# Kernel tuning notes

Measured on AMD Instinct MI355X. Metric: run time of the kernel, lower is better.

Reference implementation:

```python
import jax, jax.numpy as jnp
import numpy as np

LAMBDA = 0.1   # lambda_ init arg
RHO = 1.0      # ADMM penalty parameter
N_ITERS = 50   # fixed ADMM iteration count (replaces eps_rel/eps_abs stopping rule, jit-friendly)


def _admm_box_qp(Q1, P):
    """Solve, for every (b, n): min_x 0.5 x^T Q1[b] x + P[b,n]^T x  s.t. 0 <= x <= 1.
    Q1: [b, m, m] (shared across n, so factor once per b), P: [b, n, m]. Returns z: [b, n, m]."""
    b, n, m = P.shape
    M_inv = jnp.linalg.inv(Q1 + RHO * jnp.eye(m, dtype=Q1.dtype))  # [b, m, m]

    x0 = jnp.zeros((b, n, m), P.dtype)

    def step(carry, _):
        x, z, u = carry
        rhs = RHO * (z - u) - P                       # [b, n, m]
        x = jnp.einsum('bij,bnj->bni', M_inv, rhs)    # x-update: (Q1 + rho I) x = rhs
        z = jnp.clip(x + u, 0.0, 1.0)                 # z-update: projection onto box [lb, ub] = [0, 1]
        u = u + x - z                                 # dual update
        return (x, z, u), None

    (x, z, u), _ = jax.lax.scan(step, (x0, x0, x0), None, length=N_ITERS)
    return z


def reference(Q, V):
    b, n, d = Q.shape
    m = V.shape[1]
    V = V / m
    # Q1 = 2 V V^T : [b, m, m]
    Q1 = 2.0 * jnp.einsum('bmd,bkd->bmk', V, V)
    # P = -2 V Q^T + lambda/m : [b, n, m]  (avoid materializing the b*n stacked copies of Q1)
    P = -2.0 * jnp.einsum('bmd,bnd->bnm', V, Q) + LAMBDA / m
    x = _admm_box_qp(Q1, P)                           # [b, n, m] in [0, 1]
    xb = jnp.where(x > 0.5, 1.0, 0.0)                 # hard threshold
    coeffs = xb / (jnp.abs(xb).sum(axis=-1, keepdims=True) + 1e-10)
    return jnp.einsum('bnm,bmd->bnd', coeffs, V)


def setup_inputs() -> dict:
    key = jax.random.key(0)
    kq, kv = jax.random.split(key)
    Q = jax.random.normal(kq, (8, 2048, 128), dtype=jnp.float32)
    V = jax.random.normal(kv, (8, 128, 128), dtype=jnp.float32)
    return {"Q": Q, "V": V}
```

## Files before the change

### kernel.cpp

```cpp
#include <hip/hip_runtime.h>

#define NBATCH 8
#define NROWS 2048
#define MDIM 128
#define NITER 50
#define PSTR 65
#define RSTR_R 136
#define WSTR 104
#define XSTR 132

#define RH_B 0
#define RM_B 17408
#define RL_B 34816
#define WH_B 52224
#define WM_B 78848
#define WL_B 105472
#define CNT_B 132096
#define SMEM_BYTES 136192
#define PMAT_B 0
#define QST_B 68608
#define XB_B 0
#define CF_B 36864

typedef unsigned short ushort_t;
typedef __attribute__((ext_vector_type(8))) short bf16x8;
typedef __attribute__((ext_vector_type(8))) unsigned short us8;
typedef __attribute__((ext_vector_type(4))) unsigned short us4;
typedef __attribute__((ext_vector_type(4))) float f32x4;

__device__ __host__ __forceinline__ ushort_t f2bf(float f) {
  unsigned int u = __builtin_bit_cast(unsigned int, f);
  unsigned int r = (u + 0x7fffu + ((u >> 16) & 1u)) >> 16;
  return (ushort_t)r;
}
__device__ __forceinline__ float bf2f(ushort_t h) {
  unsigned int u = ((unsigned int)h) << 16;
  return __builtin_bit_cast(float, u);
}

__global__ __launch_bounds__(256) void mk_m64(const float* __restrict__ V,
                                              double* __restrict__ M,
                                              double* __restrict__ X0) {
  __shared__ double sA[32][130];
  __shared__ double sB[32][130];
  const int b = blockIdx.x >> 4, t = blockIdx.x & 15;
  const int i0 = (t >> 2) << 5, j0 = (t & 3) << 5;
  const float* Vb = V + b * MDIM * MDIM;
  const int tid = threadIdx.x;
  const double S = 1.0 / 128.0;
  for (int idx = tid; idx < 1024; idx += 256) {
    const int r = idx >> 5, c4 = (idx & 31) << 2;
    float4 v = *(const float4*)(Vb + (i0 + r) * MDIM + c4);
    sA[r][c4 + 0] = v.x * S; sA[r][c4 + 1] = v.y * S;
    sA[r][c4 + 2] = v.z * S; sA[r][c4 + 3] = v.w * S;
    float4 w = *(const float4*)(Vb + (j0 + r) * MDIM + c4);
    sB[r][c4 + 0] = w.x * S; sB[r][c4 + 1] = w.y * S;
    sB[r][c4 + 2] = w.z * S; sB[r][c4 + 3] = w.w * S;
  }
  __syncthreads();
  const int tx = tid & 15, ty = tid >> 4;
  double acc[2][2] = {};
  for (int k = 0; k < 128; ++k) {
    double a0 = sA[ty * 2 + 0][k], a1 = sA[ty * 2 + 1][k];
    double b0 = sB[tx * 2 + 0][k], b1 = sB[tx * 2 + 1][k];
    acc[0][0] = fma(a0, b0, acc[0][0]); acc[0][1] = fma(a0, b1, acc[0][1]);
    acc[1][0] = fma(a1, b0, acc[1][0]); acc[1][1] = fma(a1, b1, acc[1][1]);
  }
  double* Mb = M + b * 16384;
  double* Xb = X0 + b * 16384;
#pragma unroll
  for (int i = 0; i < 2; ++i)
#pragma unroll
    for (int j = 0; j < 2; ++j) {
      const int gi = i0 + ty * 2 + i, gj = j0 + tx * 2 + j;
      const double diag = (gi == gj) ? 1.0 : 0.0;
      const double mv = 2.0 * acc[i][j] + diag;
      Mb[gi * 128 + gj] = mv;
      Xb[gi * 128 + gj] = 2.0 * diag - mv;
    }
}

__global__ __launch_bounds__(256) void ns_gemm64(const double* __restrict__ A,
                                                 const double* __restrict__ B,
                                                 double* __restrict__ C,
                                                 const double* __restrict__ Xc,
                                                 int mode) {
  __shared__ double sA[32][130];
  __shared__ double sB[32][130];
  const int b = blockIdx.x >> 4, t = blockIdx.x & 15;
  const int i0 = (t >> 2) << 5, j0 = (t & 3) << 5;
  const double* Ab = A + b * 16384;
  const double* Bb = B + b * 16384;
  const int tid = threadIdx.x;
  for (int idx = tid; idx < 2048; idx += 256) {
    const int r = idx >> 6, c2 = (idx & 63) << 1;
    *(double2*)&sA[r][c2] = *(const double2*)(Ab + (i0 + r) * 128 + c2);
    *(double2*)&sB[r][c2] = *(const double2*)(Bb + (j0 + r) * 128 + c2);
  }
  __syncthreads();
  const int tx = tid & 15, ty = tid >> 4;
  double acc[2][2] = {};
  for (int k = 0; k < 128; ++k) {
    double a0 = sA[ty * 2 + 0][k], a1 = sA[ty * 2 + 1][k];
    double b0 = sB[tx * 2 + 0][k], b1 = sB[tx * 2 + 1][k];
    acc[0][0] = fma(a0, b0, acc[0][0]); acc[0][1] = fma(a0, b1, acc[0][1]);
    acc[1][0] = fma(a1, b0, acc[1][0]); acc[1][1] = fma(a1, b1, acc[1][1]);
  }
  double* Cb = C + b * 16384;
  const double* Xcb = Xc + b * 16384;
#pragma unroll
  for (int i = 0; i < 2; ++i)
#pragma unroll
    for (int j = 0; j < 2; ++j) {
      const int gi = i0 + ty * 2 + i, gj = j0 + tx * 2 + j;
      double v = acc[i][j];
      if (mode != 0) v = 2.0 * Xcb[gi * 128 + gj] - v;
      Cb[gi * 128 + gj] = v;
    }
}

__global__ __launch_bounds__(256) void prep_aux(const double* __restrict__ Minv,
                                                const float* __restrict__ V,
                                                ushort_t* __restrict__ Whg,
                                                ushort_t* __restrict__ Wmg,
                                                ushort_t* __restrict__ Wlg,
                                                double* __restrict__ VsT64) {
  const int b = blockIdx.x >> 3, ch = blockIdx.x & 7;
  const double* Mb = Minv + b * 16384;
  const float* Vb = V + b * 16384;
  ushort_t* Whb = Whg + b * 16384;
  ushort_t* Wmb = Wmg + b * 16384;
  ushort_t* Wlb = Wlg + b * 16384;
  double* Tb = VsT64 + b * 16384;
  const int base = ch * 2048;
  for (int k = threadIdx.x; k < 2048; k += 256) {
    const int idx = base + k;
    const int j = idx >> 7, c = idx & 127;
    const double diag = (j == c) ? 1.0 : 0.0;
    const float wf = (float)(diag - Mb[idx]);
    const ushort_t h = f2bf(wf);
    const float r1 = wf - bf2f(h);
    const ushort_t m_ = f2bf(r1);
    const float r2 = r1 - bf2f(m_);
    const ushort_t l_ = f2bf(r2);
    Whb[c * 128 + j] = h;
    Wmb[c * 128 + j] = m_;
    Wlb[c * 128 + j] = l_;
    Tb[idx] = (double)Vb[c * 128 + j] * (1.0 / 128.0);
  }
}

__global__ __launch_bounds__(1024) void admm_mfma(const float* __restrict__ Q,
                                                  const float* __restrict__ V,
                                                  const ushort_t* __restrict__ Whg,
                                                  const ushort_t* __restrict__ Wmg,
                                                  const ushort_t* __restrict__ Wlg,
                                                  const double* __restrict__ VsT64,
                                                  float* __restrict__ out) {
  __shared__ __align__(16) char smem[SMEM_BYTES];
  const int tid = threadIdx.x;
  const int b = blockIdx.x & 7;
  const int n0 = (blockIdx.x >> 3) << 6;
  const int lane = tid & 63;
  const int w = tid >> 6;
  const int c0_old = w << 3;
  const int c0u = __builtin_amdgcn_readfirstlane(c0_old);
  const int quad = lane >> 4, col16 = lane & 15;
  const int ct = w & 7, nh = w >> 3;
  const int rowA = ct * 16 + col16;
  const int nrow0 = (nh * 2 + 0) * 16 + col16;
  const int nrow1 = (nh * 2 + 1) * 16 + col16;
  const int cbase = ct * 16 + quad * 4;

  const float* Qb = Q + ((size_t)(b * NROWS + n0)) * MDIM;
  const double* Vtc = VsT64 + b * 16384 + c0u;
  const float* Vc = V + b * 16384 + c0u;
  float* outb = out + ((size_t)(b * NROWS + n0)) * MDIM;
  const ushort_t* WG0 = Whg + b * 16384;
  const ushort_t* WG1 = Wmg + b * 16384;
  const ushort_t* WG2 = Wlg + b * 16384;

  float* QST = (float*)(smem + QST_B);
  double* pmat = (double*)(smem + PMAT_B);
  ushort_t* rhp = (ushort_t*)(smem + RH_B);
  ushort_t* rmp = (ushort_t*)(smem + RM_B);
  ushort_t* rlp = (ushort_t*)(smem + RL_B);
  ushort_t* wh = (ushort_t*)(smem + WH_B);
  ushort_t* wm = (ushort_t*)(smem + WM_B);
  ushort_t* wl = (ushort_t*)(smem + WL_B);
  float* sCnt = (float*)(smem + CNT_B);

  for (int idx = tid; idx < 2048; idx += 1024) {
    const int r = idx >> 5, d4 = (idx & 31) << 2;
    const float4 q = *(const float4*)(Qb + r * 128 + d4);
    QST[(d4 + 0) * PSTR + r] = q.x;
    QST[(d4 + 1) * PSTR + r] = q.y;
    QST[(d4 + 2) * PSTR + r] = q.z;
    QST[(d4 + 3) * PSTR + r] = q.w;
  }
  __syncthreads();

  double p8[8];
#pragma unroll
  for (int c = 0; c < 8; ++c) p8[c] = 0.0;
  for (int d = 0; d < 128; ++d) {
    const double a = (double)QST[d * PSTR + lane];
    const double* vt = Vtc + d * 128;
#pragma unroll
    for (int c = 0; c < 8; ++c) p8[c] = fma(a, vt[c], p8[c]);
  }
  const double LAM = 0.1 / 128.0;
#pragma unroll
  for (int c = 0; c < 8; ++c) p8[c] = fma(-2.0, p8[c], LAM);
  __syncthreads();
#pragma unroll
  for (int c = 0; c < 8; ++c) pmat[lane * 128 + c0_old + c] = p8[c];
  __syncthreads();

  double pC[2][4];
#pragma unroll
  for (int i = 0; i < 4; ++i) {
    pC[0][i] = pmat[nrow0 * 128 + cbase + i];
    pC[1][i] = pmat[nrow1 * 128 + cbase + i];
  }
  __syncthreads();

  {
    const ushort_t* wg[3] = {WG0, WG1, WG2};
    ushort_t* wd[3] = {wh, wm, wl};
#pragma unroll
    for (int L = 0; L < 3; ++L)
      for (int idx = tid; idx < 1536; idx += 1024) {
        const int c = idx / 12, t8 = idx - c * 12;
        *(us8*)(wd[L] + c * WSTR + t8 * 8) =
            *(const us8*)(wg[L] + c * 128 + 32 + t8 * 8);
      }
  }
  bf16x8 wf0h = *(const bf16x8*)(WG0 + rowA * 128 + quad * 8);
  bf16x8 wf0m = *(const bf16x8*)(WG1 + rowA * 128 + quad * 8);
  bf16x8 wf0l = *(const bf16x8*)(WG2 + rowA * 128 + quad * 8);
  __syncthreads();

  double z[2][4], u[2][4];
#pragma unroll
  for (int t = 0; t < 2; ++t)
#pragma unroll
    for (int i = 0; i < 4; ++i) { z[t][i] = 0.0; u[t][i] = 0.0; }

  for (int it = 0; it < NITER; ++it) {
#pragma unroll
    for (int t = 0; t < 2; ++t) {
      const int nr = t ? nrow1 : nrow0;
      us4 hh, mm2, ll;
#pragma unroll
      for (int i = 0; i < 4; ++i) {
        const double rv = (z[t][i] - u[t][i]) - pC[t][i];
        const float rf = (float)rv;
        const ushort_t h = f2bf(rf);
        const float r1 = rf - bf2f(h);
        const ushort_t m_ = f2bf(r1);
        const float r2 = r1 - bf2f(m_);
        const ushort_t l_ = f2bf(r2);
        hh[i] = h; mm2[i] = m_; ll[i] = l_;
      }
      *(us4*)(rhp + nr * RSTR_R + cbase) = hh;
      *(us4*)(rmp + nr * RSTR_R + cbase) = mm2;
      *(us4*)(rlp + nr * RSTR_R + cbase) = ll;
    }
    __syncthreads();

    f32x4 acc0 = {0.f, 0.f, 0.f, 0.f};
    f32x4 acc1 = {0.f, 0.f, 0.f, 0.f};
#pragma unroll
    for (int ks = 0; ks < 4; ++ks) {
      bf16x8 ah, am2, al2;
      if (ks == 0) {
        ah = wf0h; am2 = wf0m; al2 = wf0l;
      } else {
        const int ko = (ks - 1) * 32 + quad * 8;
        ah  = *(const bf16x8*)(wh + rowA * WSTR + ko);
        am2 = *(const bf16x8*)(wm + rowA * WSTR + ko);
        al2 = *(const bf16x8*)(wl + rowA * WSTR + ko);
      }
      const int kq = ks * 32 + quad * 8;
      const bf16x8 b0h = *(const bf16x8*)(rhp + nrow0 * RSTR_R + kq);
      const bf16x8 b0m = *(const bf16x8*)(rmp + nrow0 * RSTR_R + kq);
      const bf16x8 b0l = *(const bf16x8*)(rlp + nrow0 * RSTR_R + kq);
      const bf16x8 b1h = *(const bf16x8*)(rhp + nrow1 * RSTR_R + kq);
      const bf16x8 b1m = *(const bf16x8*)(rmp + nrow1 * RSTR_R + kq);
      const bf16x8 b1l = *(const bf16x8*)(rlp + nrow1 * RSTR_R + kq);
      acc0 = __builtin_amdgcn_mfma_f32_16x16x32_bf16(ah,  b0h, acc0, 0, 0, 0);
      acc0 = __builtin_amdgcn_mfma_f32_16x16x32_bf16(ah,  b0m, acc0, 0, 0, 0);
      acc0 = __builtin_amdgcn_mfma_f32_16x16x32_bf16(am2, b0h, acc0, 0, 0, 0);
      acc0 = __builtin_amdgcn_mfma_f32_16x16x32_bf16(am2, b0m, acc0, 0, 0, 0);
      acc0 = __builtin_amdgcn_mfma_f32_16x16x32_bf16(ah,  b0l, acc0, 0, 0, 0);
      acc0 = __builtin_amdgcn_mfma_f32_16x16x32_bf16(al2, b0h, acc0, 0, 0, 0);
      acc1 = __builtin_amdgcn_mfma_f32_16x16x32_bf16(ah,  b1h, acc1, 0, 0, 0);
      acc1 = __builtin_amdgcn_mfma_f32_16x16x32_bf16(ah,  b1m, acc1, 0, 0, 0);
      acc1 = __builtin_amdgcn_mfma_f32_16x16x32_bf16(am2, b1h, acc1, 0, 0, 0);
      acc1 = __builtin_amdgcn_mfma_f32_16x16x32_bf16(am2, b1m, acc1, 0, 0, 0);
      acc1 = __builtin_amdgcn_mfma_f32_16x16x32_bf16(ah,  b1l, acc1, 0, 0, 0);
      acc1 = __builtin_amdgcn_mfma_f32_16x16x32_bf16(al2, b1h, acc1, 0, 0, 0);
    }
    __syncthreads();

#pragma unroll
    for (int t = 0; t < 2; ++t)
#pragma unroll
      for (int i = 0; i < 4; ++i) {
        const float corr = (t == 0) ? acc0[i] : acc1[i];
        const double rv = (z[t][i] - u[t][i]) - pC[t][i];
        const double x = rv - (double)corr;
        const double y = x + u[t][i];
        const double zn = fmin(fmax(y, 0.0), 1.0);
        u[t][i] = y - zn;
        z[t][i] = zn;
      }
  }

  float* xbm = (float*)(smem + XB_B);
#pragma unroll
  for (int t = 0; t < 2; ++t) {
    const int nr = t ? nrow1 : nrow0;
    float4 o;
    o.x = (z[t][0] > 0.5) ? 1.f : 0.f;
    o.y = (z[t][1] > 0.5) ? 1.f : 0.f;
    o.z = (z[t][2] > 0.5) ? 1.f : 0.f;
    o.w = (z[t][3] > 0.5) ? 1.f : 0.f;
    *(float4*)(xbm + nr * XSTR + cbase) = o;
  }
  __syncthreads();

  float xb8[8];
  {
    const float4 a = *(const float4*)(xbm + lane * XSTR + c0_old + 0);
    const float4 c2 = *(const float4*)(xbm + lane * XSTR + c0_old + 4);
    xb8[0] = a.x; xb8[1] = a.y; xb8[2] = a.z; xb8[3] = a.w;
    xb8[4] = c2.x; xb8[5] = c2.y; xb8[6] = c2.z; xb8[7] = c2.w;
  }
  double cnt = 0.0;
#pragma unroll
  for (int c = 0; c < 8; ++c) cnt += (double)xb8[c];
  sCnt[w * 64 + lane] = (float)cnt;
  __syncthreads();
  double k = 0.0;
#pragma unroll
  for (int g = 0; g < 16; ++g) k += (double)sCnt[g * 64 + lane];
  const double rkS = (1.0 / 128.0) / (k + 1e-10);
  float* cf = (float*)(smem + CF_B);
  {
    float4 w0, w1;
    w0.x = (float)((double)xb8[0] * rkS); w0.y = (float)((double)xb8[1] * rkS);
    w0.z = (float)((double)xb8[2] * rkS); w0.w = (float)((double)xb8[3] * rkS);
    w1.x = (float)((double)xb8[4] * rkS); w1.y = (float)((double)xb8[5] * rkS);
    w1.z = (float)((double)xb8[6] * rkS); w1.w = (float)((double)xb8[7] * rkS);
    *(float4*)(cf + lane * XSTR + c0_old + 0) = w0;
    *(float4*)(cf + lane * XSTR + c0_old + 4) = w1;
  }
  __syncthreads();

  float oa[8];
#pragma unroll
  for (int c = 0; c < 8; ++c) oa[c] = 0.f;
#pragma unroll 4
  for (int m4 = 0; m4 < 32; ++m4) {
    const float4 a4 = *(const float4*)(cf + lane * XSTR + (m4 << 2));
    const float* v0 = Vc + ((m4 << 2) + 0) * 128;
    const float* v1 = Vc + ((m4 << 2) + 1) * 128;
    const float* v2 = Vc + ((m4 << 2) + 2) * 128;
    const float* v3 = Vc + ((m4 << 2) + 3) * 128;
#pragma unroll
    for (int c = 0; c < 8; ++c) oa[c] = fmaf(a4.x, v0[c], oa[c]);
#pragma unroll
    for (int c = 0; c < 8; ++c) oa[c] = fmaf(a4.y, v1[c], oa[c]);
#pragma unroll
    for (int c = 0; c < 8; ++c) oa[c] = fmaf(a4.z, v2[c], oa[c]);
#pragma unroll
    for (int c = 0; c < 8; ++c) oa[c] = fmaf(a4.w, v3[c], oa[c]);
  }
#pragma unroll
  for (int q = 0; q < 2; ++q) {
    float4 o;
    o.x = oa[q * 4 + 0]; o.y = oa[q * 4 + 1];
    o.z = oa[q * 4 + 2]; o.w = oa[q * 4 + 3];
    *(float4*)(outb + lane * 128 + c0_old + q * 4) = o;
  }
}

extern "C" void kernel_launch(void* const* d_in, const int* in_sizes, int n_in,
                              void* d_out, int out_size, void* d_ws, size_t ws_size,
                              hipStream_t stream) {
  const float* Q = (const float*)d_in[0];
  const float* V = (const float*)d_in[1];
  float* out = (float*)d_out;
  double* ws = (double*)d_ws;
  double* Mw = ws;
  double* Xa = ws + 131072;
  double* Xb = ws + 262144;
  double* Tw = ws + 393216;

  mk_m64<<<128, 256, 0, stream>>>(V, Mw, Xa);
  double* pa = Xa;
  double* pb = Xb;
  for (int i = 0; i < 3; ++i) {
    ns_gemm64<<<128, 256, 0, stream>>>(pa, Mw, Tw, pa, 0);
    ns_gemm64<<<128, 256, 0, stream>>>(Tw, pa, pb, pa, 1);
    double* tmp = pa; pa = pb; pb = tmp;
  }
  ushort_t* Whg = (ushort_t*)Mw;
  ushort_t* Wmg = Whg + 131072;
  ushort_t* Wlg = Whg + 262144;
  double* VsT64 = Tw;
  prep_aux<<<64, 256, 0, stream>>>(pa, V, Whg, Wmg, Wlg, VsT64);
  admm_mfma<<<256, 1024, 0, stream>>>(Q, V, Whg, Wmg, Wlg, VsT64, out);
}
```

Before: 309.1 us.

## Halve ADMM block rows, keep hi/mid weight fragments in registers, shrink LDS

The main ADMM kernel now processes 32 rows per block with 512 threads (512 blocks), so each wave owns one 16-column tile over both row halves. The hi and mid bf16 weight fragments are held in registers across all k-steps, and only the low part stays in LDS, cutting shared memory from about 136KB to about 55KB so several blocks can share a CU. The small fp64 Newton-Schulz and M-build GEMMs use 16-row tiles with twice as many blocks to fill more CUs. In exchange there is higher register pressure (launch bounds 512,4), less reuse of the A fragments per block, and more redundant weight loads across blocks.

```diff
diff --git a/kernel.cpp b/kernel.cpp
--- a/kernel.cpp
+++ b/kernel.cpp
@@ -4,23 +4,21 @@
 #define NROWS 2048
 #define MDIM 128
 #define NITER 50
-#define PSTR 65
+#define PSTR2 33
 #define RSTR_R 136
-#define WSTR 104
+#define WLSTR 104
 #define XSTR 132
 
 #define RH_B 0
-#define RM_B 17408
-#define RL_B 34816
-#define WH_B 52224
-#define WM_B 78848
-#define WL_B 105472
-#define CNT_B 132096
-#define SMEM_BYTES 136192
+#define RM_B 8704
+#define RL_B 17408
+#define WL_B 26112
+#define CNT_B 52736
+#define SMEM_BYTES 54784
 #define PMAT_B 0
-#define QST_B 68608
+#define QST_B 32768
 #define XB_B 0
-#define CF_B 36864
+#define CF_B 16896
 
 typedef unsigned short ushort_t;
 typedef __attribute__((ext_vector_type(8))) short bf16x8;
@@ -41,43 +39,43 @@
 __global__ __launch_bounds__(256) void mk_m64(const float* __restrict__ V,
                                               double* __restrict__ M,
                                               double* __restrict__ X0) {
-  __shared__ double sA[32][130];
+  __shared__ double sA[16][130];
   __shared__ double sB[32][130];
-  const int b = blockIdx.x >> 4, t = blockIdx.x & 15;
-  const int i0 = (t >> 2) << 5, j0 = (t & 3) << 5;
+  const int b = blockIdx.x >> 5, t = blockIdx.x & 31;
+  const int i0 = (t >> 2) << 4, j0 = (t & 3) << 5;
   const float* Vb = V + b * MDIM * MDIM;
   const int tid = threadIdx.x;
   const double S = 1.0 / 128.0;
-  for (int idx = tid; idx < 1024; idx += 256) {
+  for (int idx = tid; idx < 512; idx += 256) {
     const int r = idx >> 5, c4 = (idx & 31) << 2;
     float4 v = *(const float4*)(Vb + (i0 + r) * MDIM + c4);
     sA[r][c4 + 0] = v.x * S; sA[r][c4 + 1] = v.y * S;
     sA[r][c4 + 2] = v.z * S; sA[r][c4 + 3] = v.w * S;
+  }
+  for (int idx = tid; idx < 1024; idx += 256) {
+    const int r = idx >> 5, c4 = (idx & 31) << 2;
     float4 w = *(const float4*)(Vb + (j0 + r) * MDIM + c4);
     sB[r][c4 + 0] = w.x * S; sB[r][c4 + 1] = w.y * S;
     sB[r][c4 + 2] = w.z * S; sB[r][c4 + 3] = w.w * S;
   }
   __syncthreads();
   const int tx = tid & 15, ty = tid >> 4;
-  double acc[2][2] = {};
+  double acc0 = 0.0, acc1 = 0.0;
   for (int k = 0; k < 128; ++k) {
-    double a0 = sA[ty * 2 + 0][k], a1 = sA[ty * 2 + 1][k];
-    double b0 = sB[tx * 2 + 0][k], b1 = sB[tx * 2 + 1][k];
-    acc[0][0] = fma(a0, b0, acc[0][0]); acc[0][1] = fma(a0, b1, acc[0][1]);
-    acc[1][0] = fma(a1, b0, acc[1][0]); acc[1][1] = fma(a1, b1, acc[1][1]);
+    const double a0 = sA[ty][k];
+    const double b0 = sB[tx * 2 + 0][k], b1 = sB[tx * 2 + 1][k];
+    acc0 = fma(a0, b0, acc0); acc1 = fma(a0, b1, acc1);
   }
   double* Mb = M + b * 16384;
   double* Xb = X0 + b * 16384;
 #pragma unroll
-  for (int i = 0; i < 2; ++i)
-#pragma unroll
-    for (int j = 0; j < 2; ++j) {
-      const int gi = i0 + ty * 2 + i, gj = j0 + tx * 2 + j;
-      const double diag = (gi == gj) ? 1.0 : 0.0;
-      const double mv = 2.0 * acc[i][j] + diag;
-      Mb[gi * 128 + gj] = mv;
-      Xb[gi * 128 + gj] = 2.0 * diag - mv;
-    }
+  for (int j = 0; j < 2; ++j) {
+    const int gi = i0 + ty, gj = j0 + tx * 2 + j;
+    const double diag = (gi == gj) ? 1.0 : 0.0;
+    const double mv = 2.0 * (j ? acc1 : acc0) + diag;
+    Mb[gi * 128 + gj] = mv;
+    Xb[gi * 128 + gj] = 2.0 * diag - mv;
+  }
 }
 
 __global__ __launch_bounds__(256) void ns_gemm64(const double* __restrict__ A,
@@ -85,38 +83,38 @@
                                                  double* __restrict__ C,
                                                  const double* __restrict__ Xc,
                                                  int mode) {
-  __shared__ double sA[32][130];
+  __shared__ double sA[16][130];
   __shared__ double sB[32][130];
-  const int b = blockIdx.x >> 4, t = blockIdx.x & 15;
-  const int i0 = (t >> 2) << 5, j0 = (t & 3) << 5;
+  const int b = blockIdx.x >> 5, t = blockIdx.x & 31;
+  const int i0 = (t >> 2) << 4, j0 = (t & 3) << 5;
   const double* Ab = A + b * 16384;
   const double* Bb = B + b * 16384;
   const int tid = threadIdx.x;
+  for (int idx = tid; idx < 1024; idx += 256) {
+    const int r = idx >> 6, c2 = (idx & 63) << 1;
+    *(double2*)&sA[r][c2] = *(const double2*)(Ab + (i0 + r) * 128 + c2);
+  }
   for (int idx = tid; idx < 2048; idx += 256) {
     const int r = idx >> 6, c2 = (idx & 63) << 1;
-    *(double2*)&sA[r][c2] = *(const double2*)(Ab + (i0 + r) * 128 + c2);
     *(double2*)&sB[r][c2] = *(const double2*)(Bb + (j0 + r) * 128 + c2);
   }
   __syncthreads();
   const int tx = tid & 15, ty = tid >> 4;
-  double acc[2][2] = {};
+  double acc0 = 0.0, acc1 = 0.0;
   for (int k = 0; k < 128; ++k) {
-    double a0 = sA[ty * 2 + 0][k], a1 = sA[ty * 2 + 1][k];
-    double b0 = sB[tx * 2 + 0][k], b1 = sB[tx * 2 + 1][k];
-    acc[0][0] = fma(a0, b0, acc[0][0]); acc[0][1] = fma(a0, b1, acc[0][1]);
-    acc[1][0] = fma(a1, b0, acc[1][0]); acc[1][1] = fma(a1, b1, acc[1][1]);
+    const double a0 = sA[ty][k];
+    const double b0 = sB[tx * 2 + 0][k], b1 = sB[tx * 2 + 1][k];
+    acc0 = fma(a0, b0, acc0); acc1 = fma(a0, b1, acc1);
   }
   double* Cb = C + b * 16384;
   const double* Xcb = Xc + b * 16384;
 #pragma unroll
-  for (int i = 0; i < 2; ++i)
-#pragma unroll
-    for (int j = 0; j < 2; ++j) {
-      const int gi = i0 + ty * 2 + i, gj = j0 + tx * 2 + j;
-      double v = acc[i][j];
-      if (mode != 0) v = 2.0 * Xcb[gi * 128 + gj] - v;
-      Cb[gi * 128 + gj] = v;
-    }
+  for (int j = 0; j < 2; ++j) {
+    const int gi = i0 + ty, gj = j0 + tx * 2 + j;
+    double v = (j ? acc1 : acc0);
+    if (mode != 0) v = 2.0 * Xcb[gi * 128 + gj] - v;
+    Cb[gi * 128 + gj] = v;
+  }
 }
 
 __global__ __launch_bounds__(256) void prep_aux(const double* __restrict__ Minv,
@@ -150,31 +148,30 @@
   }
 }
 
-__global__ __launch_bounds__(1024) void admm_mfma(const float* __restrict__ Q,
-                                                  const float* __restrict__ V,
-                                                  const ushort_t* __restrict__ Whg,
-                                                  const ushort_t* __restrict__ Wmg,
-                                                  const ushort_t* __restrict__ Wlg,
-                                                  const double* __restrict__ VsT64,
-                                                  float* __restrict__ out) {
+__global__ __launch_bounds__(512, 4) void admm_mfma(const float* __restrict__ Q,
+                                                    const float* __restrict__ V,
+                                                    const ushort_t* __restrict__ Whg,
+                                                    const ushort_t* __restrict__ Wmg,
+                                                    const ushort_t* __restrict__ Wlg,
+                                                    const double* __restrict__ VsT64,
+                                                    float* __restrict__ out) {
   __shared__ __align__(16) char smem[SMEM_BYTES];
   const int tid = threadIdx.x;
   const int b = blockIdx.x & 7;
-  const int n0 = (blockIdx.x >> 3) << 6;
+  const int n0 = (blockIdx.x >> 3) << 5;
   const int lane = tid & 63;
   const int w = tid >> 6;
-  const int c0_old = w << 3;
-  const int c0u = __builtin_amdgcn_readfirstlane(c0_old);
   const int quad = lane >> 4, col16 = lane & 15;
-  const int ct = w & 7, nh = w >> 3;
-  const int rowA = ct * 16 + col16;
-  const int nrow0 = (nh * 2 + 0) * 16 + col16;
-  const int nrow1 = (nh * 2 + 1) * 16 + col16;
-  const int cbase = ct * 16 + quad * 4;
+  const int rowA = w * 16 + col16;
+  const int nrow0 = col16;
+  const int nrow1 = 16 + col16;
+  const int cbase = w * 16 + quad * 4;
+  const int row = lane & 31;
+  const int chalf = lane >> 5;
 
   const float* Qb = Q + ((size_t)(b * NROWS + n0)) * MDIM;
-  const double* Vtc = VsT64 + b * 16384 + c0u;
-  const float* Vc = V + b * 16384 + c0u;
+  const float* Vw = V + b * 16384 + w * 16;
+  const double* vtb = VsT64 + b * 16384 + w * 16;
   float* outb = out + ((size_t)(b * NROWS + n0)) * MDIM;
   const ushort_t* WG0 = Whg + b * 16384;
   const ushort_t* WG1 = Wmg + b * 16384;
@@ -185,18 +182,16 @@
   ushort_t* rhp = (ushort_t*)(smem + RH_B);
   ushort_t* rmp = (ushort_t*)(smem + RM_B);
   ushort_t* rlp = (ushort_t*)(smem + RL_B);
-  ushort_t* wh = (ushort_t*)(smem + WH_B);
-  ushort_t* wm = (ushort_t*)(smem + WM_B);
   ushort_t* wl = (ushort_t*)(smem + WL_B);
   float* sCnt = (float*)(smem + CNT_B);
 
-  for (int idx = tid; idx < 2048; idx += 1024) {
+  for (int idx = tid; idx < 1024; idx += 512) {
     const int r = idx >> 5, d4 = (idx & 31) << 2;
     const float4 q = *(const float4*)(Qb + r * 128 + d4);
-    QST[(d4 + 0) * PSTR + r] = q.x;
-    QST[(d4 + 1) * PSTR + r] = q.y;
-    QST[(d4 + 2) * PSTR + r] = q.z;
-    QST[(d4 + 3) * PSTR + r] = q.w;
+    QST[(d4 + 0) * PSTR2 + r] = q.x;
+    QST[(d4 + 1) * PSTR2 + r] = q.y;
+    QST[(d4 + 2) * PSTR2 + r] = q.z;
+    QST[(d4 + 3) * PSTR2 + r] = q.w;
   }
   __syncthreads();
 
@@ -204,17 +199,19 @@
 #pragma unroll
   for (int c = 0; c < 8; ++c) p8[c] = 0.0;
   for (int d = 0; d < 128; ++d) {
-    const double a = (double)QST[d * PSTR + lane];
-    const double* vt = Vtc + d * 128;
-#pragma unroll
-    for (int c = 0; c < 8; ++c) p8[c] = fma(a, vt[c], p8[c]);
+    const double a = (double)QST[d * PSTR2 + row];
+    const double* vt = vtb + d * 128;
+#pragma unroll
+    for (int c = 0; c < 8; ++c) {
+      const double vv = chalf ? vt[8 + c] : vt[c];
+      p8[c] = fma(a, vv, p8[c]);
+    }
   }
   const double LAM = 0.1 / 128.0;
 #pragma unroll
   for (int c = 0; c < 8; ++c) p8[c] = fma(-2.0, p8[c], LAM);
-  __syncthreads();
-#pragma unroll
-  for (int c = 0; c < 8; ++c) pmat[lane * 128 + c0_old + c] = p8[c];
+#pragma unroll
+  for (int c = 0; c < 8; ++c) pmat[row * 128 + w * 16 + chalf * 8 + c] = p8[c];
   __syncthreads();
 
   double pC[2][4];
@@ -225,20 +222,17 @@
   }
   __syncthreads();
 
-  {
-    const ushort_t* wg[3] = {WG0, WG1, WG2};
-    ushort_t* wd[3] = {wh, wm, wl};
-#pragma unroll
-    for (int L = 0; L < 3; ++L)
-      for (int idx = tid; idx < 1536; idx += 1024) {
-        const int c = idx / 12, t8 = idx - c * 12;
-        *(us8*)(wd[L] + c * WSTR + t8 * 8) =
-            *(const us8*)(wg[L] + c * 128 + 32 + t8 * 8);
-      }
-  }
-  bf16x8 wf0h = *(const bf16x8*)(WG0 + rowA * 128 + quad * 8);
-  bf16x8 wf0m = *(const bf16x8*)(WG1 + rowA * 128 + quad * 8);
-  bf16x8 wf0l = *(const bf16x8*)(WG2 + rowA * 128 + quad * 8);
+  for (int idx = tid; idx < 1536; idx += 512) {
+    const int c = idx / 12, t8 = idx - c * 12;
+    *(us8*)(wl + c * WLSTR + t8 * 8) = *(const us8*)(WG2 + c * 128 + 32 + t8 * 8);
+  }
+  bf16x8 wfh[4], wfm[4];
+#pragma unroll
+  for (int ks = 0; ks < 4; ++ks) {
+    wfh[ks] = *(const bf16x8*)(WG0 + rowA * 128 + ks * 32 + quad * 8);
+    wfm[ks] = *(const bf16x8*)(WG1 + rowA * 128 + ks * 32 + quad * 8);
+  }
+  const bf16x8 wf0l = *(const bf16x8*)(WG2 + rowA * 128 + quad * 8);
   __syncthreads();
 
   double z[2][4], u[2][4];
@@ -273,34 +267,34 @@
     f32x4 acc1 = {0.f, 0.f, 0.f, 0.f};
 #pragma unroll
     for (int ks = 0; ks < 4; ++ks) {
-      bf16x8 ah, am2, al2;
-      if (ks == 0) {
-        ah = wf0h; am2 = wf0m; al2 = wf0l;
-      } else {
-        const int ko = (ks - 1) * 32 + quad * 8;
-        ah  = *(const bf16x8*)(wh + rowA * WSTR + ko);
-        am2 = *(const bf16x8*)(wm + rowA * WSTR + ko);
-        al2 = *(const bf16x8*)(wl + rowA * WSTR + ko);
+      const bf16x8 ah = wfh[ks];
+      const bf16x8 am2 = wfm[ks];
+      const bf16x8 al2 = (ks == 0)
+          ? wf0l
+          : *(const bf16x8*)(wl + rowA * WLSTR + (ks - 1) * 32 + quad * 8);
+      const int kq = ks * 32 + quad * 8;
+      {
+        const bf16x8 bh = *(const bf16x8*)(rhp + nrow0 * RSTR_R + kq);
+        const bf16x8 bm = *(const bf16x8*)(rmp + nrow0 * RSTR_R + kq);
+        const bf16x8 bl = *(const bf16x8*)(rlp + nrow0 * RSTR_R + kq);
+        acc0 = __builtin_amdgcn_mfma_f32_16x16x32_bf16(ah,  bh, acc0, 0, 0, 0);
+        acc0 = __builtin_amdgcn_mfma_f32_16x16x32_bf16(ah,  bm, acc0, 0, 0, 0);
+        acc0 = __builtin_amdgcn_mfma_f32_16x16x32_bf16(am2, bh, acc0, 0, 0, 0);
+        acc0 = __builtin_amdgcn_mfma_f32_16x16x32_bf16(am2, bm, acc0, 0, 0, 0);
+        acc0 = __builtin_amdgcn_mfma_f32_16x16x32_bf16(ah,  bl, acc0, 0, 0, 0);
+        acc0 = __builtin_amdgcn_mfma_f32_16x16x32_bf16(al2, bh, acc0, 0, 0, 0);
       }
-      const int kq = ks * 32 + quad * 8;
-      const bf16x8 b0h = *(const bf16x8*)(rhp + nrow0 * RSTR_R + kq);
-      const bf16x8 b0m = *(const bf16x8*)(rmp + nrow0 * RSTR_R + kq);
-      const bf16x8 b0l = *(const bf16x8*)(rlp + nrow0 * RSTR_R + kq);
-      const bf16x8 b1h = *(const bf16x8*)(rhp + nrow1 * RSTR_R + kq);
-      const bf16x8 b1m = *(const bf16x8*)(rmp + nrow1 * RSTR_R + kq);
-      const bf16x8 b1l = *(const bf16x8*)(rlp + nrow1 * RSTR_R + kq);
-      acc0 = __builtin_amdgcn_mfma_f32_16x16x32_bf16(ah,  b0h, acc0, 0, 0, 0);
-      acc0 = __builtin_amdgcn_mfma_f32_16x16x32_bf16(ah,  b0m, acc0, 0, 0, 0);
-      acc0 = __builtin_amdgcn_mfma_f32_16x16x32_bf16(am2, b0h, acc0, 0, 0, 0);
-      acc0 = __builtin_amdgcn_mfma_f32_16x16x32_bf16(am2, b0m, acc0, 0, 0, 0);
-      acc0 = __builtin_amdgcn_mfma_f32_16x16x32_bf16(ah,  b0l, acc0, 0, 0, 0);
-      acc0 = __builtin_amdgcn_mfma_f32_16x16x32_bf16(al2, b0h, acc0, 0, 0, 0);
-      acc1 = __builtin_amdgcn_mfma_f32_16x16x32_bf16(ah,  b1h, acc1, 0, 0, 0);
-      acc1 = __builtin_amdgcn_mfma_f32_16x16x32_bf16(ah,  b1m, acc1, 0, 0, 0);
-      acc1 = __builtin_amdgcn_mfma_f32_16x16x32_bf16(am2, b1h, acc1, 0, 0, 0);
-      acc1 = __builtin_amdgcn_mfma_f32_16x16x32_bf16(am2, b1m, acc1, 0, 0, 0);
-      acc1 = __builtin_amdgcn_mfma_f32_16x16x32_bf16(ah,  b1l, acc1, 0, 0, 0);
-      acc1 = __builtin_amdgcn_mfma_f32_16x16x32_bf16(al2, b1h, acc1, 0, 0, 0);
+      {
+        const bf16x8 bh = *(const bf16x8*)(rhp + nrow1 * RSTR_R + kq);
+        const bf16x8 bm = *(const bf16x8*)(rmp + nrow1 * RSTR_R + kq);
+        const bf16x8 bl = *(const bf16x8*)(rlp + nrow1 * RSTR_R + kq);
+        acc1 = __builtin_amdgcn_mfma_f32_16x16x32_bf16(ah,  bh, acc1, 0, 0, 0);
+        acc1 = __builtin_amdgcn_mfma_f32_16x16x32_bf16(ah,  bm, acc1, 0, 0, 0);
+        acc1 = __builtin_amdgcn_mfma_f32_16x16x32_bf16(am2, bh, acc1, 0, 0, 0);
+        acc1 = __builtin_amdgcn_mfma_f32_16x16x32_bf16(am2, bm, acc1, 0, 0, 0);
+        acc1 = __builtin_amdgcn_mfma_f32_16x16x32_bf16(ah,  bl, acc1, 0, 0, 0);
+        acc1 = __builtin_amdgcn_mfma_f32_16x16x32_bf16(al2, bh, acc1, 0, 0, 0);
+      }
     }
     __syncthreads();
 
@@ -331,21 +325,22 @@
   }
   __syncthreads();
 
+  const int c8 = w * 16 + chalf * 8;
   float xb8[8];
   {
-    const float4 a = *(const float4*)(xbm + lane * XSTR + c0_old + 0);
-    const float4 c2 = *(const float4*)(xbm + lane * XSTR + c0_old + 4);
+    const float4 a = *(const float4*)(xbm + row * XSTR + c8 + 0);
+    const float4 c2 = *(const float4*)(xbm + row * XSTR + c8 + 4);
     xb8[0] = a.x; xb8[1] = a.y; xb8[2] = a.z; xb8[3] = a.w;
     xb8[4] = c2.x; xb8[5] = c2.y; xb8[6] = c2.z; xb8[7] = c2.w;
   }
   double cnt = 0.0;
 #pragma unroll
   for (int c = 0; c < 8; ++c) cnt += (double)xb8[c];
-  sCnt[w * 64 + lane] = (float)cnt;
+  sCnt[(w * 2 + chalf) * 32 + row] = (float)cnt;
   __syncthreads();
   double k = 0.0;
 #pragma unroll
-  for (int g = 0; g < 16; ++g) k += (double)sCnt[g * 64 + lane];
+  for (int g = 0; g < 16; ++g) k += (double)sCnt[g * 32 + row];
   const double rkS = (1.0 / 128.0) / (k + 1e-10);
   float* cf = (float*)(smem + CF_B);
   {
@@ -354,8 +349,8 @@
     w0.z = (float)((double)xb8[2] * rkS); w0.w = (float)((double)xb8[3] * rkS);
     w1.x = (float)((double)xb8[4] * rkS); w1.y = (float)((double)xb8[5] * rkS);
     w1.z = (float)((double)xb8[6] * rkS); w1.w = (float)((double)xb8[7] * rkS);
-    *(float4*)(cf + lane * XSTR + c0_old + 0) = w0;
-    *(float4*)(cf + lane * XSTR + c0_old + 4) = w1;
+    *(float4*)(cf + row * XSTR + c8 + 0) = w0;
+    *(float4*)(cf + row * XSTR + c8 + 4) = w1;
   }
   __syncthreads();
 
@@ -364,26 +359,25 @@
   for (int c = 0; c < 8; ++c) oa[c] = 0.f;
 #pragma unroll 4
   for (int m4 = 0; m4 < 32; ++m4) {
-    const float4 a4 = *(const float4*)(cf + lane * XSTR + (m4 << 2));
-    const float* v0 = Vc + ((m4 << 2) + 0) * 128;
-    const float* v1 = Vc + ((m4 << 2) + 1) * 128;
-    const float* v2 = Vc + ((m4 << 2) + 2) * 128;
-    const float* v3 = Vc + ((m4 << 2) + 3) * 128;
-#pragma unroll
-    for (int c = 0; c < 8; ++c) oa[c] = fmaf(a4.x, v0[c], oa[c]);
-#pragma unroll
-    for (int c = 0; c < 8; ++c) oa[c] = fmaf(a4.y, v1[c], oa[c]);
-#pragma unroll
-    for (int c = 0; c < 8; ++c) oa[c] = fmaf(a4.z, v2[c], oa[c]);
-#pragma unroll
-    for (int c = 0; c < 8; ++c) oa[c] = fmaf(a4.w, v3[c], oa[c]);
+    const float4 a4 = *(const float4*)(cf + row * XSTR + (m4 << 2));
+#pragma unroll
+    for (int mm = 0; mm < 4; ++mm) {
+      const int m = (m4 << 2) + mm;
+      const float* vp = Vw + m * 128;
+      const float am = (mm == 0) ? a4.x : (mm == 1) ? a4.y : (mm == 2) ? a4.z : a4.w;
+#pragma unroll
+      for (int c = 0; c < 8; ++c) {
+        const float vv = chalf ? vp[8 + c] : vp[c];
+        oa[c] = fmaf(am, vv, oa[c]);
+      }
+    }
   }
 #pragma unroll
   for (int q = 0; q < 2; ++q) {
     float4 o;
     o.x = oa[q * 4 + 0]; o.y = oa[q * 4 + 1];
     o.z = oa[q * 4 + 2]; o.w = oa[q * 4 + 3];
-    *(float4*)(outb + lane * 128 + c0_old + q * 4) = o;
+    *(float4*)(outb + row * 128 + c8 + q * 4) = o;
   }
 }
 
@@ -399,12 +393,12 @@
   double* Xb = ws + 262144;
   double* Tw = ws + 393216;
 
-  mk_m64<<<128, 256, 0, stream>>>(V, Mw, Xa);
+  mk_m64<<<256, 256, 0, stream>>>(V, Mw, Xa);
   double* pa = Xa;
   double* pb = Xb;
   for (int i = 0; i < 3; ++i) {
-    ns_gemm64<<<128, 256, 0, stream>>>(pa, Mw, Tw, pa, 0);
-    ns_gemm64<<<128, 256, 0, stream>>>(Tw, pa, pb, pa, 1);
+    ns_gemm64<<<256, 256, 0, stream>>>(pa, Mw, Tw, pa, 0);
+    ns_gemm64<<<256, 256, 0, stream>>>(Tw, pa, pb, pa, 1);
     double* tmp = pa; pa = pb; pb = tmp;
   }
   ushort_t* Whg = (ushort_t*)Mw;
@@ -412,5 +406,5 @@
   ushort_t* Wlg = Whg + 262144;
   double* VsT64 = Tw;
   prep_aux<<<64, 256, 0, stream>>>(pa, V, Whg, Wmg, Wlg, VsT64);
-  admm_mfma<<<256, 1024, 0, stream>>>(Q, V, Whg, Wmg, Wlg, VsT64, out);
-}
+  admm_mfma<<<512, 512, 0, stream>>>(Q, V, Whg, Wmg, Wlg, VsT64, out);
+}
```

Result: slower. 323.6 us (+4.7%).
